# Performance work log

Measured on AMD Instinct MI355X. Metric: run time of the kernel, lower is better.

## Reference

```python
import jax, jax.numpy as jnp
import numpy as np

B, F, D, OUT = 1024, 256, 256, 128
EXP = [10, 25]          # expansion_rates
CUM = [1, 10]           # cum_expansion_rates


def setup_inputs() -> dict:
    key = jax.random.key(0)
    ks = jax.random.split(key, 12)
    s = 0.05
    return {
        "h0": jax.random.normal(ks[0], (B, 1, F), jnp.float32),
        "h1": jax.random.normal(ks[1], (B, EXP[0], F), jnp.float32),
        "h2": jax.random.normal(ks[2], (B, EXP[0] * EXP[1], F), jnp.float32),
        "mask0": (jax.random.uniform(ks[3], (B, 1, EXP[0], 1)) < 0.9).astype(jnp.float32),
        "mask1": (jax.random.uniform(ks[4], (B, EXP[0], EXP[1], 1)) < 0.9).astype(jnp.float32),
        "W_self0": jax.random.normal(ks[5], (D, F), jnp.float32) * s,
        "W_neigh0": jax.random.normal(ks[6], (D, F), jnp.float32) * s,
        "W_pool0": jax.random.normal(ks[7], (D, D), jnp.float32) * s,
        "W_self1": jax.random.normal(ks[8], (D, 2 * D), jnp.float32) * s,
        "W_neigh1": jax.random.normal(ks[9], (D, 2 * D), jnp.float32) * s,
        "W_pool1": jax.random.normal(ks[10], (D, D), jnp.float32) * s,
        "W_out": jax.random.normal(ks[11], (OUT, 2 * D), jnp.float32) * s,
    }


def _sage_layer(x_self, x_neigh, mask, Ws, Wn, Wp):
    # x_self: (B, P, Fin), x_neigh: (B, P, S, Fin), mask: (B, P, S, 1)
    h_self = x_self @ Ws.T                                  # (B, P, D)
    h_neigh = jax.nn.relu(x_neigh @ Wn.T) * mask            # (B, P, S, D)
    h_pool = jnp.max(h_neigh, axis=-2) @ Wp.T               # (B, P, D) -- max pooling
    return jnp.concatenate([h_self, h_pool], axis=-1)       # (B, P, 2D)


def reference(h0, h1, h2, mask0, mask1,
              W_self0, W_neigh0, W_pool0,
              W_self1, W_neigh1, W_pool1, W_out):
    states = [h0, h1, h2]
    masks = [mask0, mask1]
    layers = [(W_self0, W_neigh0, W_pool0), (W_self1, W_neigh1, W_pool1)]
    layer_input_sizes = [F, 2 * D]
    depth = 2
    for i, (Ws, Wn, Wp) in enumerate(layers):
        fin = layer_input_sizes[i]
        for j in range(depth - i):
            x_self = states[j]
            x_neigh = states[j + 1].reshape(-1, CUM[j], EXP[j], fin)
            m = masks[j].reshape(-1, CUM[j], EXP[j], 1)
            states[j] = _sage_layer(x_self, x_neigh, m, Ws, Wn, Wp)
    return states[0][:, 0] @ W_out.T  # (B, OUT)
```

## Files before the change

kernel.cpp:

```cpp
#include <hip/hip_runtime.h>


typedef __bf16 bf16_t;
typedef bf16_t bf16x8 __attribute__((ext_vector_type(8)));
typedef float  f32x4  __attribute__((ext_vector_type(4)));

__device__ inline bf16x8 cvt8(const float4 a, const float4 b) {
  bf16x8 t;
  t[0]=(bf16_t)a.x; t[1]=(bf16_t)a.y; t[2]=(bf16_t)a.z; t[3]=(bf16_t)a.w;
  t[4]=(bf16_t)b.x; t[5]=(bf16_t)b.y; t[6]=(bf16_t)b.z; t[7]=(bf16_t)b.w;
  return t;
}

__global__ __launch_bounds__(256) void cvt_bf16(
    const float* __restrict__ s, bf16_t* __restrict__ d, int n) {
  const int i = (blockIdx.x * 256 + threadIdx.x) * 8;
  if (i < n) {
    const float4 a = *(const float4*)(s + i);
    const float4 b = *(const float4*)(s + i + 4);
    *(bf16x8*)(d + i) = cvt8(a, b);
  }
}

__device__ inline void gload_lds16(const bf16_t* g, bf16x8* l) {
  __builtin_amdgcn_global_load_lds(
      (const __attribute__((address_space(1))) unsigned int*)g,
      (__attribute__((address_space(3))) unsigned int*)l, 16, 0, 0);
}

template<typename AT> struct PreA {
  float4 lo, hi;
  __device__ void fetch(const AT* p) { lo = *(const float4*)p; hi = *(const float4*)(p + 4); }
  __device__ bf16x8 get() const { return cvt8(lo, hi); }
};
template<> struct PreA<bf16_t> {
  bf16x8 v;
  __device__ void fetch(const bf16_t* p) { v = *(const bf16x8*)p; }
  __device__ bf16x8 get() const { return v; }
};

template<int S, int PR, int P, int K, typename AT>
__global__ __launch_bounds__(256) void pool_mfma(
    const AT* __restrict__ A, const bf16_t* __restrict__ W,
    const float* __restrict__ mask, bf16_t* __restrict__ out)
{
  constexpr int ROWS = P * PR;
  constexpr int PM   = ROWS / 16;
  constexpr int MTP  = PR / 16;
  constexpr int T    = K / 32;
  __shared__ bf16x8 Blds[2][1024];
  __shared__ bf16x8 Alds[2][ROWS * 4];
  __shared__ float  mlds[ROWS];

  const int tid  = threadIdx.x;
  const int lane = tid & 63, wv = tid >> 6, quad = lane >> 4, lrow = lane & 15;
  const long p0  = (long)blockIdx.x * P;

  if (tid < P * S) mlds[(tid / S) * PR + (tid % S)] = mask[p0 * S + tid];

  const bf16_t* wptr[4];
#pragma unroll
  for (int j = 0; j < 4; ++j) {
    const int n = ((tid >> 6) + j * 4) * 16 + (tid & 15);
    wptr[j] = W + (long)n * K + ((tid >> 4) & 3) * 8;
  }
  const int wbase = (tid >> 6) * 64;

  const int mr = (tid >> 6) * 16 + (tid & 15);
  const int pp = mr / PR, rr = mr % PR;
  const long grow = (p0 + pp) * (long)S + (rr < S ? rr : S - 1);
  const AT* aptr = A + grow * (long)K + ((tid >> 4) & 3) * 8;

  f32x4 acc[PM][4];
#pragma unroll
  for (int pm = 0; pm < PM; ++pm)
#pragma unroll
    for (int nl = 0; nl < 4; ++nl) acc[pm][nl] = (f32x4){0.f, 0.f, 0.f, 0.f};

  PreA<AT> a0, apre[2];
  a0.fetch(aptr);
#pragma unroll
  for (int j = 0; j < 4; ++j) gload_lds16(wptr[j], &Blds[0][wbase + j * 256]);
  apre[0].fetch(aptr + 32);
  apre[1].fetch(aptr + 64);
  Alds[0][tid] = a0.get();
  __syncthreads();

#pragma unroll
  for (int i = 0; i < T; ++i) {
    const int cur = i & 1, nxt = cur ^ 1;
    if (i + 1 < T) {
#pragma unroll
      for (int j = 0; j < 4; ++j)
        gload_lds16(wptr[j] + (i + 1) * 32, &Blds[nxt][wbase + j * 256]);
    }
    bf16x8 bfr[4];
#pragma unroll
    for (int nl = 0; nl < 4; ++nl)
      bfr[nl] = Blds[cur][((wv * 4 + nl) * 4 + quad) * 16 + lrow];
#pragma unroll
    for (int pm = 0; pm < PM; ++pm) {
      const bf16x8 afr = Alds[cur][(pm * 4 + quad) * 16 + lrow];
#pragma unroll
      for (int nl = 0; nl < 4; ++nl)
        acc[pm][nl] = __builtin_amdgcn_mfma_f32_16x16x32_bf16(
            afr, bfr[nl], acc[pm][nl], 0, 0, 0);
    }
    if (i + 1 < T) {
      Alds[nxt][tid] = apre[i & 1].get();
      if (i + 3 < T) apre[i & 1].fetch(aptr + (i + 3) * 32);
      __syncthreads();
    }
  }

#pragma unroll
  for (int p = 0; p < P; ++p) {
#pragma unroll
    for (int nl = 0; nl < 4; ++nl) {
      float m = 0.f;
#pragma unroll
      for (int mt = 0; mt < MTP; ++mt) {
        const f32x4 v = acc[p * MTP + mt][nl];
#pragma unroll
        for (int reg = 0; reg < 4; ++reg) {
          const int row = mt * 16 + quad * 4 + reg;
          if (row < S)
            m = fmaxf(m, fmaxf(v[reg], 0.f) * mlds[p * PR + row]);
        }
      }
      m = fmaxf(m, __shfl_xor(m, 16));
      m = fmaxf(m, __shfl_xor(m, 32));
      if (lane < 16)
        out[(p0 + p) * 256 + wv * 64 + nl * 16 + lrow] = (bf16_t)m;
    }
  }
}

template<int MT, int N, int K, typename OT>
__global__ __launch_bounds__(256) void plain_mfma(
    const bf16_t* __restrict__ A0, const bf16_t* __restrict__ W0, int c0,
    const bf16_t* __restrict__ A1, const bf16_t* __restrict__ W1, int c1,
    OT* __restrict__ out, int ldc)
{
  constexpr int NTW    = N / 64;
  constexpr int BSLOTS = N * 4;
  constexpr int BPT    = BSLOTS / 256;
  constexpr int ROWS   = MT * 16;
  constexpr int ASLOTS = ROWS * 4;
  constexpr int T      = K / 32;
  __shared__ bf16x8 Blds[2][BSLOTS];
  __shared__ bf16x8 Alds[2][ASLOTS];

  const bf16_t* __restrict__ A = blockIdx.y ? A1 : A0;
  const bf16_t* __restrict__ W = blockIdx.y ? W1 : W0;
  const int coff = blockIdx.y ? c1 : c0;

  const int tid  = threadIdx.x;
  const int lane = tid & 63, wv = tid >> 6, quad = lane >> 4, lrow = lane & 15;
  const long r0  = (long)blockIdx.x * ROWS;

  const bf16_t* wptr[BPT];
#pragma unroll
  for (int j = 0; j < BPT; ++j) {
    const int n = ((tid >> 6) + j * 4) * 16 + (tid & 15);
    wptr[j] = W + (long)n * K + ((tid >> 4) & 3) * 8;
  }
  const int wbase = (tid >> 6) * 64;

  const bool aact = tid < ASLOTS;
  const int  mr   = (tid >> 6) * 16 + (tid & 15);
  const bf16_t* aptr = A + (aact ? (r0 + mr) * (long)K + ((tid >> 4) & 3) * 8 : 0);

  f32x4 acc[MT][NTW];
#pragma unroll
  for (int mt = 0; mt < MT; ++mt)
#pragma unroll
    for (int nl = 0; nl < NTW; ++nl) acc[mt][nl] = (f32x4){0.f, 0.f, 0.f, 0.f};

  PreA<bf16_t> a0p, apre[2];
  if (aact) a0p.fetch(aptr);
#pragma unroll
  for (int j = 0; j < BPT; ++j) gload_lds16(wptr[j], &Blds[0][wbase + j * 256]);
  if (aact) {
    apre[0].fetch(aptr + 32);
    apre[1].fetch(aptr + 64);
    Alds[0][tid] = a0p.get();
  }
  __syncthreads();

#pragma unroll
  for (int i = 0; i < T; ++i) {
    const int cur = i & 1, nxt = cur ^ 1;
    if (i + 1 < T) {
#pragma unroll
      for (int j = 0; j < BPT; ++j)
        gload_lds16(wptr[j] + (i + 1) * 32, &Blds[nxt][wbase + j * 256]);
    }
    bf16x8 bfr[NTW];
#pragma unroll
    for (int nl = 0; nl < NTW; ++nl)
      bfr[nl] = Blds[cur][((wv * NTW + nl) * 4 + quad) * 16 + lrow];
#pragma unroll
    for (int mt = 0; mt < MT; ++mt) {
      const bf16x8 afr = Alds[cur][(mt * 4 + quad) * 16 + lrow];
#pragma unroll
      for (int nl = 0; nl < NTW; ++nl)
        acc[mt][nl] = __builtin_amdgcn_mfma_f32_16x16x32_bf16(
            afr, bfr[nl], acc[mt][nl], 0, 0, 0);
    }
    if (i + 1 < T) {
      if (aact) {
        Alds[nxt][tid] = apre[i & 1].get();
        if (i + 3 < T) apre[i & 1].fetch(aptr + (i + 3) * 32);
      }
      __syncthreads();
    }
  }

#pragma unroll
  for (int mt = 0; mt < MT; ++mt)
#pragma unroll
    for (int nl = 0; nl < NTW; ++nl) {
      const f32x4 v = acc[mt][nl];
      const int col = coff + (wv * NTW + nl) * 16 + lrow;
#pragma unroll
      for (int reg = 0; reg < 4; ++reg) {
        const long row = r0 + mt * 16 + quad * 4 + reg;
        out[row * (long)ldc + col] = (OT)v[reg];
      }
    }
}

extern "C" void kernel_launch(void* const* d_in, const int* in_sizes, int n_in,
                              void* d_out, int out_size, void* d_ws, size_t ws_size,
                              hipStream_t stream) {
  const float* h0f   = (const float*)d_in[0];
  const float* h1f   = (const float*)d_in[1];
  const float* h2    = (const float*)d_in[2];
  const float* mask0 = (const float*)d_in[3];
  const float* mask1 = (const float*)d_in[4];
  const float* Wf[7] = { (const float*)d_in[5], (const float*)d_in[6],
                         (const float*)d_in[7], (const float*)d_in[8],
                         (const float*)d_in[9], (const float*)d_in[10],
                         (const float*)d_in[11] };
  const int   Wn[7]  = { 65536, 65536, 65536, 131072, 131072, 65536, 65536 };
  float* out = (float*)d_out;

  bf16_t* p = (bf16_t*)d_ws;
  bf16_t* Wb[7];
  for (int i = 0; i < 7; ++i) { Wb[i] = p; p += Wn[i]; }
  bf16_t* h0b = p;      p += 262144;
  bf16_t* h1b = p;      p += 2621440;
  bf16_t* pooled1  = p; p += 10240L * 256;
  bf16_t* states1  = p; p += 10240L * 512;
  bf16_t* pooled0  = p; p += 1024L * 256;
  bf16_t* states0  = p; p += 1024L * 512;
  bf16_t* pooled1b = p; p += 1024L * 256;
  bf16_t* states0b = p; p += 1024L * 512;

  const bf16_t *Ws0 = Wb[0], *Wn0 = Wb[1], *Wp0 = Wb[2], *Ws1 = Wb[3],
               *Wn1 = Wb[4], *Wp1 = Wb[5], *Wout = Wb[6];
  const dim3 blk(256);

  for (int i = 0; i < 7; ++i)
    hipLaunchKernelGGL(cvt_bf16, dim3(Wn[i] / 2048), blk, 0, stream, Wf[i], Wb[i], Wn[i]);
  hipLaunchKernelGGL(cvt_bf16, dim3(128),  blk, 0, stream, h0f, h0b, 262144);
  hipLaunchKernelGGL(cvt_bf16, dim3(1280), blk, 0, stream, h1f, h1b, 2621440);

  hipLaunchKernelGGL((pool_mfma<25, 32, 2, 256, float>), dim3(5120), blk, 0, stream,
                     h2, Wn0, mask1, pooled1);
  hipLaunchKernelGGL((pool_mfma<10, 16, 4, 256, bf16_t>), dim3(256), blk, 0, stream,
                     h1b, Wn0, mask0, pooled0);
  hipLaunchKernelGGL((plain_mfma<4, 256, 256, bf16_t>), dim3(160, 2), blk, 0, stream,
                     h1b, Ws0, 0, pooled1, Wp0, 256, states1, 512);
  hipLaunchKernelGGL((plain_mfma<1, 256, 256, bf16_t>), dim3(64, 2), blk, 0, stream,
                     h0b, Ws0, 0, pooled0, Wp0, 256, states0, 512);
  hipLaunchKernelGGL((pool_mfma<10, 16, 4, 512, bf16_t>), dim3(256), blk, 0, stream,
                     states1, Wn1, mask0, pooled1b);
  hipLaunchKernelGGL((plain_mfma<1, 256, 512, bf16_t>), dim3(64, 1), blk, 0, stream,
                     states0, Ws1, 0, states0, Ws1, 0, states0b, 512);
  hipLaunchKernelGGL((plain_mfma<1, 256, 256, bf16_t>), dim3(64, 1), blk, 0, stream,
                     pooled1b, Wp1, 256, pooled1b, Wp1, 256, states0b, 512);
  hipLaunchKernelGGL((plain_mfma<1, 128, 512, float>), dim3(64, 1), blk, 0, stream,
                     states0b, Wout, 0, states0b, Wout, 0, out, 128);
}
```

Before: 539.4 us.

## Drop LDS staging in MFMA kernels, load fragments directly; fuse conversions

Replaces the LDS double-buffered GEMM kernels with versions where each lane loads its MFMA A/B fragments straight from global memory into registers, with a two-deep register prefetch and no __syncthreads. The nine separate fp32-to-bf16 conversion launches are merged into one segmented kernel, and the mask is read from global memory instead of shared memory. Tile shapes for the plain GEMMs change and launch bounds request two blocks per CU. The aim is to remove LDS traffic, barriers and launch overhead, but weights are now re-read per wave from global memory and cache, with no sharing through LDS, and register pressure rises.

```diff
diff --git a/kernel.cpp b/kernel.cpp
--- a/kernel.cpp
+++ b/kernel.cpp
@@ -10,22 +10,6 @@
   t[0]=(bf16_t)a.x; t[1]=(bf16_t)a.y; t[2]=(bf16_t)a.z; t[3]=(bf16_t)a.w;
   t[4]=(bf16_t)b.x; t[5]=(bf16_t)b.y; t[6]=(bf16_t)b.z; t[7]=(bf16_t)b.w;
   return t;
-}
-
-__global__ __launch_bounds__(256) void cvt_bf16(
-    const float* __restrict__ s, bf16_t* __restrict__ d, int n) {
-  const int i = (blockIdx.x * 256 + threadIdx.x) * 8;
-  if (i < n) {
-    const float4 a = *(const float4*)(s + i);
-    const float4 b = *(const float4*)(s + i + 4);
-    *(bf16x8*)(d + i) = cvt8(a, b);
-  }
-}
-
-__device__ inline void gload_lds16(const bf16_t* g, bf16x8* l) {
-  __builtin_amdgcn_global_load_lds(
-      (const __attribute__((address_space(1))) unsigned int*)g,
-      (__attribute__((address_space(3))) unsigned int*)l, 16, 0, 0);
 }
 
 template<typename AT> struct PreA {
@@ -39,37 +23,45 @@
   __device__ bf16x8 get() const { return v; }
 };
 
+struct CvtArgs { const float* src[9]; int start[9]; };
+
+__global__ __launch_bounds__(256) void cvt_all(CvtArgs a, bf16_t* __restrict__ dst) {
+  const int i = (blockIdx.x * 256 + threadIdx.x) * 8;
+  int seg = 0;
+#pragma unroll
+  for (int s = 1; s < 9; ++s) if (i >= a.start[s]) seg = s;
+  const float* src = a.src[seg] + (i - a.start[seg]);
+  const float4 lo = *(const float4*)src;
+  const float4 hi = *(const float4*)(src + 4);
+  *(bf16x8*)(dst + i) = cvt8(lo, hi);
+}
+
 template<int S, int PR, int P, int K, typename AT>
-__global__ __launch_bounds__(256) void pool_mfma(
+__global__ __launch_bounds__(256, 2) void pool_direct(
     const AT* __restrict__ A, const bf16_t* __restrict__ W,
     const float* __restrict__ mask, bf16_t* __restrict__ out)
 {
-  constexpr int ROWS = P * PR;
-  constexpr int PM   = ROWS / 16;
-  constexpr int MTP  = PR / 16;
-  constexpr int T    = K / 32;
-  __shared__ bf16x8 Blds[2][1024];
-  __shared__ bf16x8 Alds[2][ROWS * 4];
-  __shared__ float  mlds[ROWS];
-
+  constexpr int PM  = (P * PR) / 16;
+  constexpr int MTP = PR / 16;
+  constexpr int T   = K / 32;
   const int tid  = threadIdx.x;
   const int lane = tid & 63, wv = tid >> 6, quad = lane >> 4, lrow = lane & 15;
   const long p0  = (long)blockIdx.x * P;
 
-  if (tid < P * S) mlds[(tid / S) * PR + (tid % S)] = mask[p0 * S + tid];
-
-  const bf16_t* wptr[4];
-#pragma unroll
-  for (int j = 0; j < 4; ++j) {
-    const int n = ((tid >> 6) + j * 4) * 16 + (tid & 15);
-    wptr[j] = W + (long)n * K + ((tid >> 4) & 3) * 8;
-  }
-  const int wbase = (tid >> 6) * 64;
-
-  const int mr = (tid >> 6) * 16 + (tid & 15);
-  const int pp = mr / PR, rr = mr % PR;
-  const long grow = (p0 + pp) * (long)S + (rr < S ? rr : S - 1);
-  const AT* aptr = A + grow * (long)K + ((tid >> 4) & 3) * 8;
+  const AT* aptr[PM];
+#pragma unroll
+  for (int pm = 0; pm < PM; ++pm) {
+    const int mr = pm * 16 + lrow;
+    const int pp = mr / PR, rr = mr % PR;
+    const long grow = (p0 + pp) * (long)S + (rr < S ? rr : S - 1);
+    aptr[pm] = A + grow * (long)K + quad * 8;
+  }
+  const bf16_t* bptr[4];
+#pragma unroll
+  for (int nl = 0; nl < 4; ++nl) {
+    const int n = (wv * 4 + nl) * 16 + lrow;
+    bptr[nl] = W + (long)n * K + quad * 8;
+  }
 
   f32x4 acc[PM][4];
 #pragma unroll
@@ -77,44 +69,46 @@
 #pragma unroll
     for (int nl = 0; nl < 4; ++nl) acc[pm][nl] = (f32x4){0.f, 0.f, 0.f, 0.f};
 
-  PreA<AT> a0, apre[2];
-  a0.fetch(aptr);
-#pragma unroll
-  for (int j = 0; j < 4; ++j) gload_lds16(wptr[j], &Blds[0][wbase + j * 256]);
-  apre[0].fetch(aptr + 32);
-  apre[1].fetch(aptr + 64);
-  Alds[0][tid] = a0.get();
-  __syncthreads();
+  PreA<AT> abuf[2][PM];
+  bf16x8   bbuf[2][4];
+#pragma unroll
+  for (int pm = 0; pm < PM; ++pm) { abuf[0][pm].fetch(aptr[pm]); abuf[1][pm].fetch(aptr[pm] + 32); }
+#pragma unroll
+  for (int nl = 0; nl < 4; ++nl)  { bbuf[0][nl] = *(const bf16x8*)bptr[nl];
+                                    bbuf[1][nl] = *(const bf16x8*)(bptr[nl] + 32); }
 
 #pragma unroll
   for (int i = 0; i < T; ++i) {
-    const int cur = i & 1, nxt = cur ^ 1;
-    if (i + 1 < T) {
-#pragma unroll
-      for (int j = 0; j < 4; ++j)
-        gload_lds16(wptr[j] + (i + 1) * 32, &Blds[nxt][wbase + j * 256]);
-    }
-    bf16x8 bfr[4];
-#pragma unroll
-    for (int nl = 0; nl < 4; ++nl)
-      bfr[nl] = Blds[cur][((wv * 4 + nl) * 4 + quad) * 16 + lrow];
-#pragma unroll
-    for (int pm = 0; pm < PM; ++pm) {
-      const bf16x8 afr = Alds[cur][(pm * 4 + quad) * 16 + lrow];
+    const int cur = i & 1;
+    bf16x8 afr[PM], bfr[4];
+#pragma unroll
+    for (int pm = 0; pm < PM; ++pm) afr[pm] = abuf[cur][pm].get();
+#pragma unroll
+    for (int nl = 0; nl < 4; ++nl)  bfr[nl] = bbuf[cur][nl];
+    if (i + 2 < T) {
+#pragma unroll
+      for (int pm = 0; pm < PM; ++pm) abuf[cur][pm].fetch(aptr[pm] + (i + 2) * 32);
+#pragma unroll
+      for (int nl = 0; nl < 4; ++nl)  bbuf[cur][nl] = *(const bf16x8*)(bptr[nl] + (i + 2) * 32);
+    }
+#pragma unroll
+    for (int pm = 0; pm < PM; ++pm)
 #pragma unroll
       for (int nl = 0; nl < 4; ++nl)
         acc[pm][nl] = __builtin_amdgcn_mfma_f32_16x16x32_bf16(
-            afr, bfr[nl], acc[pm][nl], 0, 0, 0);
-    }
-    if (i + 1 < T) {
-      Alds[nxt][tid] = apre[i & 1].get();
-      if (i + 3 < T) apre[i & 1].fetch(aptr + (i + 3) * 32);
-      __syncthreads();
-    }
+            afr[pm], bfr[nl], acc[pm][nl], 0, 0, 0);
   }
 
 #pragma unroll
   for (int p = 0; p < P; ++p) {
+    float mv[MTP][4];
+#pragma unroll
+    for (int mt = 0; mt < MTP; ++mt)
+#pragma unroll
+      for (int reg = 0; reg < 4; ++reg) {
+        const int row = mt * 16 + quad * 4 + reg;
+        mv[mt][reg] = (row < S) ? mask[(p0 + p) * S + row] : 0.f;
+      }
 #pragma unroll
     for (int nl = 0; nl < 4; ++nl) {
       float m = 0.f;
@@ -122,103 +116,79 @@
       for (int mt = 0; mt < MTP; ++mt) {
         const f32x4 v = acc[p * MTP + mt][nl];
 #pragma unroll
-        for (int reg = 0; reg < 4; ++reg) {
-          const int row = mt * 16 + quad * 4 + reg;
-          if (row < S)
-            m = fmaxf(m, fmaxf(v[reg], 0.f) * mlds[p * PR + row]);
-        }
+        for (int reg = 0; reg < 4; ++reg)
+          m = fmaxf(m, fmaxf(v[reg], 0.f) * mv[mt][reg]);
       }
       m = fmaxf(m, __shfl_xor(m, 16));
       m = fmaxf(m, __shfl_xor(m, 32));
       if (lane < 16)
-        out[(p0 + p) * 256 + wv * 64 + nl * 16 + lrow] = (bf16_t)m;
-    }
-  }
-}
-
-template<int MT, int N, int K, typename OT>
-__global__ __launch_bounds__(256) void plain_mfma(
+        out[(p0 + p) * 256 + (wv * 4 + nl) * 16 + lrow] = (bf16_t)m;
+    }
+  }
+}
+
+template<int MTW, int NTW, int N, int K, typename OT>
+__global__ __launch_bounds__(64 * (N / (16 * NTW))) void plain_direct(
     const bf16_t* __restrict__ A0, const bf16_t* __restrict__ W0, int c0,
     const bf16_t* __restrict__ A1, const bf16_t* __restrict__ W1, int c1,
     OT* __restrict__ out, int ldc)
 {
-  constexpr int NTW    = N / 64;
-  constexpr int BSLOTS = N * 4;
-  constexpr int BPT    = BSLOTS / 256;
-  constexpr int ROWS   = MT * 16;
-  constexpr int ASLOTS = ROWS * 4;
-  constexpr int T      = K / 32;
-  __shared__ bf16x8 Blds[2][BSLOTS];
-  __shared__ bf16x8 Alds[2][ASLOTS];
-
+  constexpr int T = K / 32;
   const bf16_t* __restrict__ A = blockIdx.y ? A1 : A0;
   const bf16_t* __restrict__ W = blockIdx.y ? W1 : W0;
   const int coff = blockIdx.y ? c1 : c0;
 
   const int tid  = threadIdx.x;
   const int lane = tid & 63, wv = tid >> 6, quad = lane >> 4, lrow = lane & 15;
-  const long r0  = (long)blockIdx.x * ROWS;
-
-  const bf16_t* wptr[BPT];
-#pragma unroll
-  for (int j = 0; j < BPT; ++j) {
-    const int n = ((tid >> 6) + j * 4) * 16 + (tid & 15);
-    wptr[j] = W + (long)n * K + ((tid >> 4) & 3) * 8;
-  }
-  const int wbase = (tid >> 6) * 64;
-
-  const bool aact = tid < ASLOTS;
-  const int  mr   = (tid >> 6) * 16 + (tid & 15);
-  const bf16_t* aptr = A + (aact ? (r0 + mr) * (long)K + ((tid >> 4) & 3) * 8 : 0);
-
-  f32x4 acc[MT][NTW];
-#pragma unroll
-  for (int mt = 0; mt < MT; ++mt)
+  const long r0  = (long)blockIdx.x * (MTW * 16);
+
+  const bf16_t* aptr[MTW];
+#pragma unroll
+  for (int mt = 0; mt < MTW; ++mt)
+    aptr[mt] = A + (r0 + mt * 16 + lrow) * (long)K + quad * 8;
+  const bf16_t* bptr[NTW];
+#pragma unroll
+  for (int nl = 0; nl < NTW; ++nl)
+    bptr[nl] = W + (long)((wv * NTW + nl) * 16 + lrow) * K + quad * 8;
+
+  f32x4 acc[MTW][NTW];
+#pragma unroll
+  for (int mt = 0; mt < MTW; ++mt)
 #pragma unroll
     for (int nl = 0; nl < NTW; ++nl) acc[mt][nl] = (f32x4){0.f, 0.f, 0.f, 0.f};
 
-  PreA<bf16_t> a0p, apre[2];
-  if (aact) a0p.fetch(aptr);
-#pragma unroll
-  for (int j = 0; j < BPT; ++j) gload_lds16(wptr[j], &Blds[0][wbase + j * 256]);
-  if (aact) {
-    apre[0].fetch(aptr + 32);
-    apre[1].fetch(aptr + 64);
-    Alds[0][tid] = a0p.get();
-  }
-  __syncthreads();
+  bf16x8 abuf[2][MTW], bbuf[2][NTW];
+#pragma unroll
+  for (int mt = 0; mt < MTW; ++mt) { abuf[0][mt] = *(const bf16x8*)aptr[mt];
+                                     abuf[1][mt] = *(const bf16x8*)(aptr[mt] + 32); }
+#pragma unroll
+  for (int nl = 0; nl < NTW; ++nl) { bbuf[0][nl] = *(const bf16x8*)bptr[nl];
+                                     bbuf[1][nl] = *(const bf16x8*)(bptr[nl] + 32); }
 
 #pragma unroll
   for (int i = 0; i < T; ++i) {
-    const int cur = i & 1, nxt = cur ^ 1;
-    if (i + 1 < T) {
-#pragma unroll
-      for (int j = 0; j < BPT; ++j)
-        gload_lds16(wptr[j] + (i + 1) * 32, &Blds[nxt][wbase + j * 256]);
-    }
-    bf16x8 bfr[NTW];
-#pragma unroll
-    for (int nl = 0; nl < NTW; ++nl)
-      bfr[nl] = Blds[cur][((wv * NTW + nl) * 4 + quad) * 16 + lrow];
-#pragma unroll
-    for (int mt = 0; mt < MT; ++mt) {
-      const bf16x8 afr = Alds[cur][(mt * 4 + quad) * 16 + lrow];
+    const int cur = i & 1;
+    bf16x8 afr[MTW], bfr[NTW];
+#pragma unroll
+    for (int mt = 0; mt < MTW; ++mt) afr[mt] = abuf[cur][mt];
+#pragma unroll
+    for (int nl = 0; nl < NTW; ++nl) bfr[nl] = bbuf[cur][nl];
+    if (i + 2 < T) {
+#pragma unroll
+      for (int mt = 0; mt < MTW; ++mt) abuf[cur][mt] = *(const bf16x8*)(aptr[mt] + (i + 2) * 32);
+#pragma unroll
+      for (int nl = 0; nl < NTW; ++nl) bbuf[cur][nl] = *(const bf16x8*)(bptr[nl] + (i + 2) * 32);
+    }
+#pragma unroll
+    for (int mt = 0; mt < MTW; ++mt)
 #pragma unroll
       for (int nl = 0; nl < NTW; ++nl)
         acc[mt][nl] = __builtin_amdgcn_mfma_f32_16x16x32_bf16(
-            afr, bfr[nl], acc[mt][nl], 0, 0, 0);
-    }
-    if (i + 1 < T) {
-      if (aact) {
-        Alds[nxt][tid] = apre[i & 1].get();
-        if (i + 3 < T) apre[i & 1].fetch(aptr + (i + 3) * 32);
-      }
-      __syncthreads();
-    }
-  }
-
-#pragma unroll
-  for (int mt = 0; mt < MT; ++mt)
+            afr[mt], bfr[nl], acc[mt][nl], 0, 0, 0);
+  }
+
+#pragma unroll
+  for (int mt = 0; mt < MTW; ++mt)
 #pragma unroll
     for (int nl = 0; nl < NTW; ++nl) {
       const f32x4 v = acc[mt][nl];
@@ -239,48 +209,48 @@
   const float* h2    = (const float*)d_in[2];
   const float* mask0 = (const float*)d_in[3];
   const float* mask1 = (const float*)d_in[4];
-  const float* Wf[7] = { (const float*)d_in[5], (const float*)d_in[6],
-                         (const float*)d_in[7], (const float*)d_in[8],
-                         (const float*)d_in[9], (const float*)d_in[10],
-                         (const float*)d_in[11] };
-  const int   Wn[7]  = { 65536, 65536, 65536, 131072, 131072, 65536, 65536 };
   float* out = (float*)d_out;
 
+  const int sz[9] = { 65536, 65536, 65536, 131072, 131072, 65536, 65536,
+                      262144, 2621440 };
+  CvtArgs ca;
+  ca.src[0] = (const float*)d_in[5];  ca.src[1] = (const float*)d_in[6];
+  ca.src[2] = (const float*)d_in[7];  ca.src[3] = (const float*)d_in[8];
+  ca.src[4] = (const float*)d_in[9];  ca.src[5] = (const float*)d_in[10];
+  ca.src[6] = (const float*)d_in[11]; ca.src[7] = h0f; ca.src[8] = h1f;
   bf16_t* p = (bf16_t*)d_ws;
-  bf16_t* Wb[7];
-  for (int i = 0; i < 7; ++i) { Wb[i] = p; p += Wn[i]; }
-  bf16_t* h0b = p;      p += 262144;
-  bf16_t* h1b = p;      p += 2621440;
-  bf16_t* pooled1  = p; p += 10240L * 256;
-  bf16_t* states1  = p; p += 10240L * 512;
-  bf16_t* pooled0  = p; p += 1024L * 256;
-  bf16_t* states0  = p; p += 1024L * 512;
-  bf16_t* pooled1b = p; p += 1024L * 256;
-  bf16_t* states0b = p; p += 1024L * 512;
-
-  const bf16_t *Ws0 = Wb[0], *Wn0 = Wb[1], *Wp0 = Wb[2], *Ws1 = Wb[3],
-               *Wn1 = Wb[4], *Wp1 = Wb[5], *Wout = Wb[6];
+  bf16_t* seg[9];
+  { int off = 0;
+    for (int i = 0; i < 9; ++i) { ca.start[i] = off; seg[i] = p + off; off += sz[i]; } }
+  const bf16_t *Ws0 = seg[0], *Wn0 = seg[1], *Wp0 = seg[2], *Ws1 = seg[3],
+               *Wn1 = seg[4], *Wp1 = seg[5], *Wout = seg[6],
+               *h0b = seg[7], *h1b = seg[8];
+  bf16_t* q = p + 3473408;
+  bf16_t* pooled1  = q; q += 10240L * 256;
+  bf16_t* states1  = q; q += 10240L * 512;
+  bf16_t* pooled0  = q; q += 1024L * 256;
+  bf16_t* states0  = q; q += 1024L * 512;
+  bf16_t* pooled1b = q; q += 1024L * 256;
+  bf16_t* states0b = q; q += 1024L * 512;
+
   const dim3 blk(256);
 
-  for (int i = 0; i < 7; ++i)
-    hipLaunchKernelGGL(cvt_bf16, dim3(Wn[i] / 2048), blk, 0, stream, Wf[i], Wb[i], Wn[i]);
-  hipLaunchKernelGGL(cvt_bf16, dim3(128),  blk, 0, stream, h0f, h0b, 262144);
-  hipLaunchKernelGGL(cvt_bf16, dim3(1280), blk, 0, stream, h1f, h1b, 2621440);
-
-  hipLaunchKernelGGL((pool_mfma<25, 32, 2, 256, float>), dim3(5120), blk, 0, stream,
+  hipLaunchKernelGGL(cvt_all, dim3(1696), blk, 0, stream, ca, p);
+
+  hipLaunchKernelGGL((pool_direct<25, 32, 2, 256, float>), dim3(5120), blk, 0, stream,
                      h2, Wn0, mask1, pooled1);
-  hipLaunchKernelGGL((pool_mfma<10, 16, 4, 256, bf16_t>), dim3(256), blk, 0, stream,
+  hipLaunchKernelGGL((pool_direct<10, 16, 4, 256, bf16_t>), dim3(256), blk, 0, stream,
                      h1b, Wn0, mask0, pooled0);
-  hipLaunchKernelGGL((plain_mfma<4, 256, 256, bf16_t>), dim3(160, 2), blk, 0, stream,
+  hipLaunchKernelGGL((plain_direct<2, 4, 256, 256, bf16_t>), dim3(320, 2), blk, 0, stream,
                      h1b, Ws0, 0, pooled1, Wp0, 256, states1, 512);
-  hipLaunchKernelGGL((plain_mfma<1, 256, 256, bf16_t>), dim3(64, 2), blk, 0, stream,
+  hipLaunchKernelGGL((plain_direct<1, 4, 256, 256, bf16_t>), dim3(64, 2), blk, 0, stream,
                      h0b, Ws0, 0, pooled0, Wp0, 256, states0, 512);
-  hipLaunchKernelGGL((pool_mfma<10, 16, 4, 512, bf16_t>), dim3(256), blk, 0, stream,
+  hipLaunchKernelGGL((pool_direct<10, 16, 4, 512, bf16_t>), dim3(256), blk, 0, stream,
                      states1, Wn1, mask0, pooled1b);
-  hipLaunchKernelGGL((plain_mfma<1, 256, 512, bf16_t>), dim3(64, 1), blk, 0, stream,
+  hipLaunchKernelGGL((plain_direct<1, 4, 256, 512, bf16_t>), dim3(64, 1), blk, 0, stream,
                      states0, Ws1, 0, states0, Ws1, 0, states0b, 512);
-  hipLaunchKernelGGL((plain_mfma<1, 256, 256, bf16_t>), dim3(64, 1), blk, 0, stream,
+  hipLaunchKernelGGL((plain_direct<1, 4, 256, 256, bf16_t>), dim3(64, 1), blk, 0, stream,
                      pooled1b, Wp1, 256, pooled1b, Wp1, 256, states0b, 512);
-  hipLaunchKernelGGL((plain_mfma<1, 128, 512, float>), dim3(64, 1), blk, 0, stream,
+  hipLaunchKernelGGL((plain_direct<1, 4, 128, 512, float>), dim3(64, 1), dim3(128), 0, stream,
                      states0b, Wout, 0, states0b, Wout, 0, out, 128);
 }
```

Result: slower. 613.5 us (+13.7%).
